# Kernel optimization log

Measured on AMD Instinct MI355X. Metric: run time of the kernel, lower is better.

Reference implementation:

```python
import jax, jax.numpy as jnp
import numpy as np

TAU = 0.5


def _l2norm(x):
    return x / jnp.linalg.norm(x, axis=1, keepdims=True)


def _project(z, W1, b1, W2, b2):
    h = jax.nn.elu(z @ W1.T + b1)
    return h @ W2.T + b2


def _semi_loss(h1, h2):
    # cos sim via row-normalized matmul
    n1 = _l2norm(h1)
    n2 = _l2norm(h2)
    between = jnp.exp((n1 @ n2.T) / TAU)  # [N, N]
    refl = jnp.exp((n1 @ n1.T) / TAU)     # [N, N]
    pos = jnp.diagonal(between)
    denom = refl.sum(axis=1) + between.sum(axis=1) + pos \
        - jnp.diagonal(refl) - jnp.diagonal(between)
    return -jnp.log(pos / denom)


def setup_inputs() -> dict:
    key = jax.random.key(0)
    k1, k2, k3, k4 = jax.random.split(key, 4)
    N, D, P = 12288, 256, 256
    z1 = jax.random.normal(k1, (N, D), dtype=jnp.float32)
    z2 = jax.random.normal(k2, (N, D), dtype=jnp.float32)
    W1 = jax.random.normal(k3, (P, D), dtype=jnp.float32) * (1.0 / np.sqrt(D))
    b1 = jnp.zeros((P,), dtype=jnp.float32)
    W2 = jax.random.normal(k4, (D, P), dtype=jnp.float32) * (1.0 / np.sqrt(P))
    b2 = jnp.zeros((D,), dtype=jnp.float32)
    return {"z1": z1, "z2": z2, "W1": W1, "b1": b1, "W2": W2, "b2": b2}


def reference(z1, z2, W1, b1, W2, b2):
    h1 = _project(z1, W1, b1, W2, b2)
    h2 = _project(z2, W1, b1, W2, b2)
    l1 = _semi_loss(h1, h2)
    l2 = _semi_loss(h2, h1)
    return ((l1 + l2) * 0.5).mean()
```

## Files before the change

kernel.cpp:

```cpp
#include <hip/hip_runtime.h>
#include <hip/hip_bf16.h>
#include <hip/hip_fp8.h>


#define NROWS 12288
#define TWO_N 24576
#define KDIM 256
#define BM 128
#define BN 128
#define BK 32
#define BJ 128
#define NTILE 192
#define PAIRS 96
#define SLOTS 16
#define FB 48
#define LOG2E 1.4426950408889634f
#define SIMSCALE 1.6986436f
#define LN2F 0.6931471805599453f

#if __has_builtin(__builtin_amdgcn_exp2f)
#define EXP2F(x) __builtin_amdgcn_exp2f(x)
#else
#define EXP2F(x) exp2f(x)
#endif

typedef __bf16 bf16x8 __attribute__((ext_vector_type(8)));
typedef __bf16 bf16x4v __attribute__((ext_vector_type(4)));
typedef float f32x4 __attribute__((ext_vector_type(4)));
typedef int i32x4 __attribute__((ext_vector_type(4)));
typedef int i32x8 __attribute__((ext_vector_type(8)));
typedef unsigned char uchar;

typedef const __attribute__((address_space(1))) void* gptr_t;
typedef __attribute__((address_space(3))) void* lptr_t;

__device__ __forceinline__ void stage_slab(const __bf16* g, int row0, int kelem,
                                           __bf16* lds, int w, int l) {
#pragma unroll
  for (int t = 0; t < 2; ++t) {
    int chunk = w * 2 + t;
    int r = chunk * 16 + (l >> 2);
    int c = l & 3;
    int src = c ^ (r & 3);
    const __bf16* ga = g + (size_t)(row0 + r) * KDIM + kelem + src * 8;
    __bf16* la = lds + chunk * 512;
    __builtin_amdgcn_global_load_lds((gptr_t)ga, (lptr_t)la, 16, 0, 0);
  }
}

__device__ __forceinline__ bf16x8 read_frag(const __bf16* lds, int rowbase,
                                            int tile, int l) {
  int r = rowbase + tile * 16 + (l & 15);
  int q = l >> 4;
  int blk = q ^ (r & 3);
  return *(const bf16x8*)(lds + r * 32 + blk * 8);
}

__device__ __forceinline__ void gemm_tile_core(const __bf16* A, int arow0,
                                               const __bf16* B, int brow0,
                                               __bf16* As, __bf16* Bs,
                                               f32x4 (&acc)[4][4], int w, int l) {
  const int warow = (w >> 1) * 64;
  const int wbrow = (w & 1) * 64;
#pragma unroll
  for (int ks = 0; ks < KDIM / BK; ++ks) {
    __syncthreads();
    stage_slab(A, arow0, ks * BK, As, w, l);
    stage_slab(B, brow0, ks * BK, Bs, w, l);
    __syncthreads();
    bf16x8 aF[4], bF[4];
#pragma unroll
    for (int mi = 0; mi < 4; ++mi) aF[mi] = read_frag(As, warow, mi, l);
#pragma unroll
    for (int ni = 0; ni < 4; ++ni) bF[ni] = read_frag(Bs, wbrow, ni, l);
#pragma unroll
    for (int mi = 0; mi < 4; ++mi)
#pragma unroll
      for (int ni = 0; ni < 4; ++ni)
        acc[mi][ni] = __builtin_amdgcn_mfma_f32_16x16x32_bf16(
            aF[mi], bF[ni], acc[mi][ni], 0, 0, 0);
  }
}

__global__ void cast_all_kernel(const float* __restrict__ z1,
                                const float* __restrict__ z2,
                                const float* __restrict__ W1,
                                const float* __restrict__ W2,
                                __bf16* __restrict__ Zb,
                                __bf16* __restrict__ W1b,
                                __bf16* __restrict__ W2b) {
  const int n4z = NROWS * KDIM / 4;
  const int n4w = KDIM * KDIM / 4;
  int i = blockIdx.x * blockDim.x + threadIdx.x;
  const float* src;
  __bf16* dst;
  int j;
  if (i < n4z) {
    src = z1; dst = Zb; j = i;
  } else if (i < 2 * n4z) {
    src = z2; dst = Zb + (size_t)NROWS * KDIM; j = i - n4z;
  } else if (i < 2 * n4z + n4w) {
    src = W1; dst = W1b; j = i - 2 * n4z;
  } else if (i < 2 * n4z + 2 * n4w) {
    src = W2; dst = W2b; j = i - 2 * n4z - n4w;
  } else {
    return;
  }
  float4 v = *(const float4*)(src + (size_t)j * 4);
  bf16x4v o;
  o[0] = (__bf16)v.x; o[1] = (__bf16)v.y; o[2] = (__bf16)v.z; o[3] = (__bf16)v.w;
  *(bf16x4v*)(dst + (size_t)j * 4) = o;
}

__global__ __launch_bounds__(256, 2) void proj1_kernel(
    const __bf16* __restrict__ Zb, const __bf16* __restrict__ W1b,
    const float* __restrict__ b1, __bf16* __restrict__ Tb) {
  __shared__ __align__(16) __bf16 As[BM * BK];
  __shared__ __align__(16) __bf16 Bs[BN * BK];
  int w = threadIdx.x >> 6, l = threadIdx.x & 63;
  int i0 = blockIdx.x * BM, j0 = blockIdx.y * BN;
  int warow = (w >> 1) * 64, wbrow = (w & 1) * 64;
  f32x4 acc[4][4] = {};
  gemm_tile_core(Zb, i0, W1b, j0, As, Bs, acc, w, l);
  float bias[4];
#pragma unroll
  for (int ni = 0; ni < 4; ++ni) bias[ni] = b1[j0 + wbrow + ni * 16 + (l & 15)];
#pragma unroll
  for (int mi = 0; mi < 4; ++mi)
#pragma unroll
    for (int ni = 0; ni < 4; ++ni)
#pragma unroll
      for (int v = 0; v < 4; ++v) {
        int row = i0 + warow + mi * 16 + (l >> 4) * 4 + v;
        int col = j0 + wbrow + ni * 16 + (l & 15);
        float x = acc[mi][ni][v] + bias[ni];
        x = x > 0.f ? x : (EXP2F(x * LOG2E) - 1.f);
        Tb[(size_t)row * KDIM + col] = (__bf16)x;
      }
}

__global__ __launch_bounds__(256, 2) void proj2_kernel(
    const __bf16* __restrict__ Tb, const __bf16* __restrict__ W2b,
    const float* __restrict__ b2, float* __restrict__ H,
    float* __restrict__ SS) {
  __shared__ __align__(16) __bf16 As[BM * BK];
  __shared__ __align__(16) __bf16 Bs[BN * BK];
  int w = threadIdx.x >> 6, l = threadIdx.x & 63;
  int i0 = blockIdx.x * BM, j0 = blockIdx.y * BN;
  int warow = (w >> 1) * 64, wbrow = (w & 1) * 64;
  f32x4 acc[4][4] = {};
  gemm_tile_core(Tb, i0, W2b, j0, As, Bs, acc, w, l);
  float bias[4];
#pragma unroll
  for (int ni = 0; ni < 4; ++ni) bias[ni] = b2[j0 + wbrow + ni * 16 + (l & 15)];
  float ss[4][4] = {};
#pragma unroll
  for (int mi = 0; mi < 4; ++mi)
#pragma unroll
    for (int ni = 0; ni < 4; ++ni)
#pragma unroll
      for (int v = 0; v < 4; ++v) {
        int row = i0 + warow + mi * 16 + (l >> 4) * 4 + v;
        int col = j0 + wbrow + ni * 16 + (l & 15);
        float x = acc[mi][ni][v] + bias[ni];
        H[(size_t)row * KDIM + col] = x;
        ss[mi][v] += x * x;
      }
#pragma unroll
  for (int mi = 0; mi < 4; ++mi)
#pragma unroll
    for (int v = 0; v < 4; ++v) {
      float x = ss[mi][v];
      x += __shfl_xor(x, 1, 64);
      x += __shfl_xor(x, 2, 64);
      x += __shfl_xor(x, 4, 64);
      x += __shfl_xor(x, 8, 64);
      if ((l & 15) == 0)
        atomicAdd(&SS[i0 + warow + mi * 16 + (l >> 4) * 4 + v], x);
    }
}

__device__ __forceinline__ unsigned int pack4_fp8(float a, float b, float c,
                                                  float d) {
#if __has_builtin(__builtin_amdgcn_cvt_pk_fp8_f32)
  int v = 0;
  v = __builtin_amdgcn_cvt_pk_fp8_f32(a, b, v, false);
  v = __builtin_amdgcn_cvt_pk_fp8_f32(c, d, v, true);
  return (unsigned int)v;
#else
  __hip_fp8_e4m3 qa(a), qb(b), qc(c), qd(d);
  return (unsigned int)qa.__x | ((unsigned int)qb.__x << 8) |
         ((unsigned int)qc.__x << 16) | ((unsigned int)qd.__x << 24);
#endif
}

__global__ void norm_kernel(const float* __restrict__ H,
                            const float* __restrict__ SS,
                            uchar* __restrict__ Nq) {
  int i = blockIdx.x * blockDim.x + threadIdx.x;
  size_t idx = (size_t)i * 8;
  if (idx >= (size_t)TWO_N * KDIM) return;
  int row = (int)(idx >> 8);
  float inv = rsqrtf(SS[row]) * SIMSCALE;
  float4 h0 = *(const float4*)(H + idx);
  float4 h1 = *(const float4*)(H + idx + 4);
  uint2 o;
  o.x = pack4_fp8(h0.x * inv, h0.y * inv, h0.z * inv, h0.w * inv);
  o.y = pack4_fp8(h1.x * inv, h1.y * inv, h1.z * inv, h1.w * inv);
  *(uint2*)(Nq + idx) = o;
}

__global__ __launch_bounds__(256, 2) void sim_kernel(
    const uchar* __restrict__ Nq, float* __restrict__ Rlow,
    float* __restrict__ Rhigh, float* __restrict__ Dsame,
    float* __restrict__ Dcross) {
  __shared__ __align__(16) uchar Bs[2][BJ * KDIM];
  int tid = threadIdx.x;
  int w = tid >> 6, l = tid & 63;
  int q = l >> 4;
  int rx = l & 15;
  int b = blockIdx.x;
  int p = b >> 4;
  int s = b & 15;
  const int I1 = p, I2 = NTILE - 1 - p;
  const int L1 = NTILE - I1;
  int fstart = (s == 0) ? 0 : 13 + (s - 1) * 12;
  int fend = fstart + ((s == 0) ? 13 : 12);
  int warow = (w >> 1) * 64;
  int wbcol = (w & 1) * 64;

  unsigned off0[8];
#pragma unroll
  for (int t = 0; t < 8; ++t) {
    int ch = w * 8 + t;
    int r = ch * 4 + (l >> 4);
    int c = l & 15;
    int src = c ^ (r & 15);
    off0[t] = (unsigned)(r * KDIM + src * 16);
  }
  auto jtile_of = [&](int F) { return (F < L1) ? (I1 + F) : (F - 1); };
  auto atile_of = [&](int F) { return (F < L1) ? I1 : I2; };

  auto stage = [&](int F, int bi) {
    unsigned jo = (unsigned)(jtile_of(F) * (BM * KDIM));
#pragma unroll
    for (int t = 0; t < 8; ++t) {
      const uchar* ga = Nq + (size_t)(jo + off0[t]);
      uchar* la = Bs[bi] + (w * 8 + t) * 1024;
      __builtin_amdgcn_global_load_lds((gptr_t)ga, (lptr_t)la, 16, 0, 0);
    }
  };

  i32x8 aF[4][2];
  auto load_aF = [&](int Atile) {
#pragma unroll
    for (int mi = 0; mi < 4; ++mi) {
      const uchar* ap = Nq +
          (size_t)(Atile * BM + warow + mi * 16 + rx) * KDIM + q * 32;
#pragma unroll
      for (int hf = 0; hf < 2; ++hf)
        aF[mi][hf] = *(const i32x8*)(ap + hf * 128);
    }
  };

  int rdo[2][2];
#pragma unroll
  for (int hf = 0; hf < 2; ++hf) {
    int kb = hf * 8 + 2 * q;
    rdo[hf][0] = (kb ^ rx) << 4;
    rdo[hf][1] = ((kb + 1) ^ rx) << 4;
  }

  f32x4 rs4[4] = {};
  f32x4 cs4[4];
  int pend = 0;
  float* pendR = nullptr;
  int pendBase = 0;

  auto flushrs = [&](int Atile, int h) {
    float* R = h ? Rhigh : Rlow;
#pragma unroll
    for (int mi = 0; mi < 4; ++mi)
#pragma unroll
      for (int v = 0; v < 4; ++v) {
        float x = rs4[mi][v];
        x += __shfl_xor(x, 1, 64);
        x += __shfl_xor(x, 2, 64);
        x += __shfl_xor(x, 4, 64);
        x += __shfl_xor(x, 8, 64);
        if (rx == 0)
          atomicAdd(&R[Atile * BM + warow + mi * 16 + q * 4 + v], x);
        rs4[mi][v] = 0.f;
      }
  };
  auto flushcs = [&]() {
#pragma unroll
    for (int nj = 0; nj < 4; ++nj) {
      float c = (cs4[nj][0] + cs4[nj][1]) + (cs4[nj][2] + cs4[nj][3]);
      c += __shfl_xor(c, 16, 64);
      c += __shfl_xor(c, 32, 64);
      if (q == 0)
        atomicAdd(&pendR[pendBase + wbcol + nj * 16 + rx], c);
    }
    pend = 0;
  };

  const f32x4 Z4 = {0.f, 0.f, 0.f, 0.f};

  int Aprev = atile_of(fstart);
  int hprev = (jtile_of(fstart) >= NTILE / 2) ? 1 : 0;
  load_aF(Aprev);
  stage(fstart, 0);

  for (int f = fstart; f < fend; ++f) {
    int bi = (f - fstart) & 1;
    __syncthreads();
    if (f + 1 < fend) stage(f + 1, bi ^ 1);
    if (pend) flushcs();

    int Atile = atile_of(f);
    int Jt = jtile_of(f);
    int h = (Jt >= NTILE / 2) ? 1 : 0;
    if (Atile != Aprev) {
      flushrs(Aprev, hprev);
      load_aF(Atile);
      Aprev = Atile;
      hprev = h;
    } else if (h != hprev) {
      flushrs(Aprev, hprev);
      hprev = h;
    }

    bool dsame = (Jt == Atile);
    bool dcross = (Jt == Atile + NTILE / 2);
    float* Rcol = (Atile >= NTILE / 2) ? Rhigh : Rlow;

    const uchar* bL = Bs[bi] + (size_t)(wbcol + rx) * KDIM;
    const uchar* p00 = bL + rdo[0][0];
    const uchar* p01 = bL + rdo[0][1];
    const uchar* p10 = bL + rdo[1][0];
    const uchar* p11 = bL + rdo[1][1];

#pragma unroll
    for (int nj = 0; nj < 4; ++nj) {
      const int no = nj * 4096;
      i32x8 bF0 = __builtin_shufflevector(*(const i32x4*)(p00 + no),
                                          *(const i32x4*)(p01 + no),
                                          0, 1, 2, 3, 4, 5, 6, 7);
      i32x8 bF1 = __builtin_shufflevector(*(const i32x4*)(p10 + no),
                                          *(const i32x4*)(p11 + no),
                                          0, 1, 2, 3, 4, 5, 6, 7);
      f32x4 acc[4];
#pragma unroll
      for (int mi = 0; mi < 4; ++mi)
        acc[mi] = __builtin_amdgcn_mfma_scale_f32_16x16x128_f8f6f4(
            aF[mi][0], bF0, Z4, 0, 0, 0, 0x7F7F7F7F, 0, 0x7F7F7F7F);
#pragma unroll
      for (int mi = 0; mi < 4; ++mi)
        acc[mi] = __builtin_amdgcn_mfma_scale_f32_16x16x128_f8f6f4(
            aF[mi][1], bF1, acc[mi], 0, 0, 0, 0x7F7F7F7F, 0, 0x7F7F7F7F);
#pragma unroll
      for (int mi = 0; mi < 4; ++mi) {
        f32x4 e4;
        e4[0] = EXP2F(acc[mi][0]);
        e4[1] = EXP2F(acc[mi][1]);
        e4[2] = EXP2F(acc[mi][2]);
        e4[3] = EXP2F(acc[mi][3]);
        rs4[mi] += e4;
        cs4[nj] = (mi == 0) ? e4 : (cs4[nj] + e4);
      }

      if (dsame | dcross) {
        float* D = dsame ? Dsame : Dcross;
#pragma unroll
        for (int mi = 0; mi < 4; ++mi)
#pragma unroll
          for (int v = 0; v < 4; ++v) {
            int li = warow + mi * 16 + q * 4 + v;
            int lj = wbcol + nj * 16 + rx;
            if (li == lj) D[Atile * BM + li] = acc[mi][v];
          }
      }
    }

    if (!dsame) {
      pend = 1;
      pendR = Rcol;
      pendBase = Jt * BM;
    }
  }

  if (pend) flushcs();
  flushrs(Aprev, hprev);
}

__global__ void finalize1_kernel(const float* __restrict__ Rlow,
                                 const float* __restrict__ Rhigh,
                                 const float* __restrict__ Dsame,
                                 const float* __restrict__ Dcross,
                                 float* __restrict__ partial) {
  __shared__ float red[256];
  int k = blockIdx.x * 256 + threadIdx.x;
  float d1 = Rlow[k] + Rhigh[k] - EXP2F(Dsame[k]);
  float d2 = Rhigh[NROWS + k] + Rlow[NROWS + k] - EXP2F(Dsame[NROWS + k]);
  float acc = 0.5f * (logf(d1) + logf(d2)) - LN2F * Dcross[k];
  red[threadIdx.x] = acc;
  __syncthreads();
  for (int s = 128; s > 0; s >>= 1) {
    if (threadIdx.x < s) red[threadIdx.x] += red[threadIdx.x + s];
    __syncthreads();
  }
  if (threadIdx.x == 0) partial[blockIdx.x] = red[0];
}

__global__ void finalize2_kernel(const float* __restrict__ partial,
                                 float* __restrict__ out) {
  float x = (threadIdx.x < FB) ? partial[threadIdx.x] : 0.f;
#pragma unroll
  for (int s = 32; s > 0; s >>= 1) x += __shfl_down(x, s, 64);
  if (threadIdx.x == 0) out[0] = x / (float)NROWS;
}

extern "C" void kernel_launch(void* const* d_in, const int* in_sizes, int n_in,
                              void* d_out, int out_size, void* d_ws,
                              size_t ws_size, hipStream_t stream) {
  const float* z1 = (const float*)d_in[0];
  const float* z2 = (const float*)d_in[1];
  const float* W1 = (const float*)d_in[2];
  const float* b1 = (const float*)d_in[3];
  const float* W2 = (const float*)d_in[4];
  const float* b2 = (const float*)d_in[5];
  float* out = (float*)d_out;

  char* ws = (char*)d_ws;
  size_t off = 0;
  auto alloc = [&](size_t bytes) -> void* {
    void* p = ws + off;
    off += (bytes + 255) & ~(size_t)255;
    return p;
  };
  __bf16* Zb   = (__bf16*)alloc((size_t)TWO_N * KDIM * 2);
  __bf16* W1b  = (__bf16*)alloc((size_t)KDIM * KDIM * 2);
  __bf16* W2b  = (__bf16*)alloc((size_t)KDIM * KDIM * 2);
  __bf16* Tb   = (__bf16*)alloc((size_t)TWO_N * KDIM * 2);
  float*  H    = (float*)alloc((size_t)TWO_N * KDIM * 4);
  float*  SS   = (float*)alloc((size_t)TWO_N * 4);
  float*  Rlow = (float*)alloc((size_t)TWO_N * 4);
  float*  Rhigh= (float*)alloc((size_t)TWO_N * 4);
  float*  Dsame= (float*)alloc((size_t)TWO_N * 4);
  float*  Dcross=(float*)alloc((size_t)NROWS * 4);
  float*  partial=(float*)alloc((size_t)FB * 4);
  uchar*  Nq = (uchar*)Zb;

  hipMemsetAsync(SS, 0, (size_t)TWO_N * 4, stream);
  hipMemsetAsync(Rlow, 0, (size_t)TWO_N * 4, stream);
  hipMemsetAsync(Rhigh, 0, (size_t)TWO_N * 4, stream);

  int n4z = NROWS * KDIM / 4;
  int n4w = KDIM * KDIM / 4;
  int n4all = 2 * n4z + 2 * n4w;
  cast_all_kernel<<<(n4all + 255) / 256, 256, 0, stream>>>(z1, z2, W1, W2, Zb,
                                                           W1b, W2b);

  proj1_kernel<<<dim3(TWO_N / BM, KDIM / BN), 256, 0, stream>>>(Zb, W1b, b1, Tb);
  proj2_kernel<<<dim3(TWO_N / BM, KDIM / BN), 256, 0, stream>>>(Tb, W2b, b2, H, SS);

  int n8n = TWO_N * KDIM / 8;
  norm_kernel<<<(n8n + 255) / 256, 256, 0, stream>>>(H, SS, Nq);

  sim_kernel<<<PAIRS * SLOTS, 256, 0, stream>>>(Nq, Rlow, Rhigh, Dsame,
                                                Dcross);
  finalize1_kernel<<<FB, 256, 0, stream>>>(Rlow, Rhigh, Dsame, Dcross, partial);
  finalize2_kernel<<<1, 64, 0, stream>>>(partial, out);
}
```

Before: 226.4 us.

## Load B fragments directly from global instead of staging through LDS

Removes the double-buffered LDS staging of the B tile (global_load_lds plus __syncthreads) in the similarity kernel and has each wave load its B fragments straight from global memory, software-prefetching the next 16-column slice into registers. It also merges three memsets into one, which relies on SS, Rlow and Rhigh being contiguous in the workspace. This drops block-wide barriers and the LDS footprint, which could raise occupancy. In exchange, B data is no longer shared across the waves of a block, so global/L2 traffic per block doubles.

```diff
diff --git a/kernel.cpp b/kernel.cpp
--- a/kernel.cpp
+++ b/kernel.cpp
@@ -9,7 +9,6 @@
 #define BM 128
 #define BN 128
 #define BK 32
-#define BJ 128
 #define NTILE 192
 #define PAIRS 96
 #define SLOTS 16
@@ -214,7 +213,6 @@
     const uchar* __restrict__ Nq, float* __restrict__ Rlow,
     float* __restrict__ Rhigh, float* __restrict__ Dsame,
     float* __restrict__ Dcross) {
-  __shared__ __align__(16) uchar Bs[2][BJ * KDIM];
   int tid = threadIdx.x;
   int w = tid >> 6, l = tid & 63;
   int q = l >> 4;
@@ -229,26 +227,19 @@
   int warow = (w >> 1) * 64;
   int wbcol = (w & 1) * 64;
 
-  unsigned off0[8];
-#pragma unroll
-  for (int t = 0; t < 8; ++t) {
-    int ch = w * 8 + t;
-    int r = ch * 4 + (l >> 4);
-    int c = l & 15;
-    int src = c ^ (r & 15);
-    off0[t] = (unsigned)(r * KDIM + src * 16);
-  }
   auto jtile_of = [&](int F) { return (F < L1) ? (I1 + F) : (F - 1); };
   auto atile_of = [&](int F) { return (F < L1) ? I1 : I2; };
 
-  auto stage = [&](int F, int bi) {
-    unsigned jo = (unsigned)(jtile_of(F) * (BM * KDIM));
-#pragma unroll
-    for (int t = 0; t < 8; ++t) {
-      const uchar* ga = Nq + (size_t)(jo + off0[t]);
-      uchar* la = Bs[bi] + (w * 8 + t) * 1024;
-      __builtin_amdgcn_global_load_lds((gptr_t)ga, (lptr_t)la, 16, 0, 0);
-    }
+  const uchar* bBase = Nq + (size_t)(wbcol + rx) * KDIM + q * 32;
+
+  auto loadB = [&](int Jt, int nj, i32x8& b0, i32x8& b1) {
+    const uchar* ptr = bBase + (size_t)Jt * (BM * KDIM) + nj * (16 * KDIM);
+    i32x4 a0 = *(const i32x4*)(ptr);
+    i32x4 a1 = *(const i32x4*)(ptr + 16);
+    i32x4 a2 = *(const i32x4*)(ptr + 128);
+    i32x4 a3 = *(const i32x4*)(ptr + 144);
+    b0 = __builtin_shufflevector(a0, a1, 0, 1, 2, 3, 4, 5, 6, 7);
+    b1 = __builtin_shufflevector(a2, a3, 0, 1, 2, 3, 4, 5, 6, 7);
   };
 
   i32x8 aF[4][2];
@@ -262,14 +253,6 @@
         aF[mi][hf] = *(const i32x8*)(ap + hf * 128);
     }
   };
-
-  int rdo[2][2];
-#pragma unroll
-  for (int hf = 0; hf < 2; ++hf) {
-    int kb = hf * 8 + 2 * q;
-    rdo[hf][0] = (kb ^ rx) << 4;
-    rdo[hf][1] = ((kb + 1) ^ rx) << 4;
-  }
 
   f32x4 rs4[4] = {};
   f32x4 cs4[4];
@@ -310,17 +293,16 @@
   int Aprev = atile_of(fstart);
   int hprev = (jtile_of(fstart) >= NTILE / 2) ? 1 : 0;
   load_aF(Aprev);
-  stage(fstart, 0);
 
   for (int f = fstart; f < fend; ++f) {
-    int bi = (f - fstart) & 1;
-    __syncthreads();
-    if (f + 1 < fend) stage(f + 1, bi ^ 1);
-    if (pend) flushcs();
-
     int Atile = atile_of(f);
     int Jt = jtile_of(f);
     int h = (Jt >= NTILE / 2) ? 1 : 0;
+
+    i32x8 b0c, b1c, b0n, b1n;
+    loadB(Jt, 0, b0c, b1c);
+
+    if (pend) flushcs();
     if (Atile != Aprev) {
       flushrs(Aprev, hprev);
       load_aF(Atile);
@@ -335,30 +317,18 @@
     bool dcross = (Jt == Atile + NTILE / 2);
     float* Rcol = (Atile >= NTILE / 2) ? Rhigh : Rlow;
 
-    const uchar* bL = Bs[bi] + (size_t)(wbcol + rx) * KDIM;
-    const uchar* p00 = bL + rdo[0][0];
-    const uchar* p01 = bL + rdo[0][1];
-    const uchar* p10 = bL + rdo[1][0];
-    const uchar* p11 = bL + rdo[1][1];
-
 #pragma unroll
     for (int nj = 0; nj < 4; ++nj) {
-      const int no = nj * 4096;
-      i32x8 bF0 = __builtin_shufflevector(*(const i32x4*)(p00 + no),
-                                          *(const i32x4*)(p01 + no),
-                                          0, 1, 2, 3, 4, 5, 6, 7);
-      i32x8 bF1 = __builtin_shufflevector(*(const i32x4*)(p10 + no),
-                                          *(const i32x4*)(p11 + no),
-                                          0, 1, 2, 3, 4, 5, 6, 7);
+      if (nj < 3) loadB(Jt, nj + 1, b0n, b1n);
       f32x4 acc[4];
 #pragma unroll
       for (int mi = 0; mi < 4; ++mi)
         acc[mi] = __builtin_amdgcn_mfma_scale_f32_16x16x128_f8f6f4(
-            aF[mi][0], bF0, Z4, 0, 0, 0, 0x7F7F7F7F, 0, 0x7F7F7F7F);
+            aF[mi][0], b0c, Z4, 0, 0, 0, 0x7F7F7F7F, 0, 0x7F7F7F7F);
 #pragma unroll
       for (int mi = 0; mi < 4; ++mi)
         acc[mi] = __builtin_amdgcn_mfma_scale_f32_16x16x128_f8f6f4(
-            aF[mi][1], bF1, acc[mi], 0, 0, 0, 0x7F7F7F7F, 0, 0x7F7F7F7F);
+            aF[mi][1], b1c, acc[mi], 0, 0, 0, 0x7F7F7F7F, 0, 0x7F7F7F7F);
 #pragma unroll
       for (int mi = 0; mi < 4; ++mi) {
         f32x4 e4;
@@ -381,6 +351,8 @@
             if (li == lj) D[Atile * BM + li] = acc[mi][v];
           }
       }
+      b0c = b0n;
+      b1c = b1n;
     }
 
     if (!dsame) {
@@ -452,9 +424,7 @@
   float*  partial=(float*)alloc((size_t)FB * 4);
   uchar*  Nq = (uchar*)Zb;
 
-  hipMemsetAsync(SS, 0, (size_t)TWO_N * 4, stream);
-  hipMemsetAsync(Rlow, 0, (size_t)TWO_N * 4, stream);
-  hipMemsetAsync(Rhigh, 0, (size_t)TWO_N * 4, stream);
+  hipMemsetAsync(SS, 0, (size_t)3 * TWO_N * 4, stream);
 
   int n4z = NROWS * KDIM / 4;
   int n4w = KDIM * KDIM / 4;
```

Result: slower. 270.2 us (+19.3%).

## Swap operand roles in sim kernel: keep column tile in registers, stream rows

Applied to the files above, without the earlier changes.

The similarity kernel now keeps the fixed tile (jbig or p) as B fragments in registers and streams the varying tiles through LDS as the A operand. The per-tile row-sum reduction moves to a deferred atomic flush, and the column sums accumulate across iterations and flush only when the tile or half changes. This is meant to cut the number of column-sum atomics and shuffle reductions, which previously happened on every tile. The three separate memsets are merged into one, which relies on SS, Rlow and Rhigh being contiguous in the workspace; each allocation is 96 KB, a multiple of 256 bytes, so no padding gaps appear.

```diff
diff --git a/kernel.cpp b/kernel.cpp
--- a/kernel.cpp
+++ b/kernel.cpp
@@ -9,7 +9,6 @@
 #define BM 128
 #define BN 128
 #define BK 32
-#define BJ 128
 #define NTILE 192
 #define PAIRS 96
 #define SLOTS 16
@@ -214,7 +213,7 @@
     const uchar* __restrict__ Nq, float* __restrict__ Rlow,
     float* __restrict__ Rhigh, float* __restrict__ Dsame,
     float* __restrict__ Dcross) {
-  __shared__ __align__(16) uchar Bs[2][BJ * KDIM];
+  __shared__ __align__(16) uchar As[2][BM * KDIM];
   int tid = threadIdx.x;
   int w = tid >> 6, l = tid & 63;
   int q = l >> 4;
@@ -222,8 +221,8 @@
   int b = blockIdx.x;
   int p = b >> 4;
   int s = b & 15;
-  const int I1 = p, I2 = NTILE - 1 - p;
-  const int L1 = NTILE - I1;
+  const int jbig = NTILE - 1 - p;
+  const int len1 = NTILE - p;
   int fstart = (s == 0) ? 0 : 13 + (s - 1) * 12;
   int fend = fstart + ((s == 0) ? 13 : 12);
   int warow = (w >> 1) * 64;
@@ -233,33 +232,31 @@
 #pragma unroll
   for (int t = 0; t < 8; ++t) {
     int ch = w * 8 + t;
-    int r = ch * 4 + (l >> 4);
-    int c = l & 15;
-    int src = c ^ (r & 15);
+    int r = ch * 4 + q;
+    int src = rx ^ (r & 15);
     off0[t] = (unsigned)(r * KDIM + src * 16);
   }
-  auto jtile_of = [&](int F) { return (F < L1) ? (I1 + F) : (F - 1); };
-  auto atile_of = [&](int F) { return (F < L1) ? I1 : I2; };
+  auto a_of = [&](int F) { return (F < len1) ? F : F - len1; };
+  auto j_of = [&](int F) { return (F < len1) ? jbig : p; };
 
   auto stage = [&](int F, int bi) {
-    unsigned jo = (unsigned)(jtile_of(F) * (BM * KDIM));
+    unsigned jo = (unsigned)(a_of(F) * (BM * KDIM));
 #pragma unroll
     for (int t = 0; t < 8; ++t) {
       const uchar* ga = Nq + (size_t)(jo + off0[t]);
-      uchar* la = Bs[bi] + (w * 8 + t) * 1024;
+      uchar* la = As[bi] + (w * 8 + t) * 1024;
       __builtin_amdgcn_global_load_lds((gptr_t)ga, (lptr_t)la, 16, 0, 0);
     }
   };
 
-  i32x8 aF[4][2];
-  auto load_aF = [&](int Atile) {
-#pragma unroll
-    for (int mi = 0; mi < 4; ++mi) {
-      const uchar* ap = Nq +
-          (size_t)(Atile * BM + warow + mi * 16 + rx) * KDIM + q * 32;
-#pragma unroll
-      for (int hf = 0; hf < 2; ++hf)
-        aF[mi][hf] = *(const i32x8*)(ap + hf * 128);
+  i32x8 bF[4][2];
+  auto load_bF = [&](int jt) {
+#pragma unroll
+    for (int nj = 0; nj < 4; ++nj) {
+      const uchar* bp =
+          Nq + (size_t)(jt * BM + wbcol + nj * 16 + rx) * KDIM + q * 32;
+      bF[nj][0] = *(const i32x8*)(bp);
+      bF[nj][1] = *(const i32x8*)(bp + 128);
     }
   };
 
@@ -272,13 +269,113 @@
   }
 
   f32x4 rs4[4] = {};
-  f32x4 cs4[4];
-  int pend = 0;
-  float* pendR = nullptr;
-  int pendBase = 0;
-
-  auto flushrs = [&](int Atile, int h) {
+  f32x4 cs4[4] = {};
+  int rpend = 0, rBase = 0;
+  float* rP = nullptr;
+
+  auto flushrs_atomic = [&]() {
+    if (rx == 0) {
+#pragma unroll
+      for (int mi = 0; mi < 4; ++mi)
+#pragma unroll
+        for (int v = 0; v < 4; ++v)
+          atomicAdd(&rP[rBase + warow + mi * 16 + q * 4 + v], rs4[mi][v]);
+    }
+#pragma unroll
+    for (int mi = 0; mi < 4; ++mi)
+      rs4[mi] = (f32x4){0.f, 0.f, 0.f, 0.f};
+    rpend = 0;
+  };
+  auto flushcs = [&](int jt, int h) {
     float* R = h ? Rhigh : Rlow;
+#pragma unroll
+    for (int nj = 0; nj < 4; ++nj) {
+      float c = (cs4[nj][0] + cs4[nj][1]) + (cs4[nj][2] + cs4[nj][3]);
+      c += __shfl_xor(c, 16, 64);
+      c += __shfl_xor(c, 32, 64);
+      if (q == 0)
+        atomicAdd(&R[jt * BM + wbcol + nj * 16 + rx], c);
+      cs4[nj] = (f32x4){0.f, 0.f, 0.f, 0.f};
+    }
+  };
+
+  const f32x4 Z4 = {0.f, 0.f, 0.f, 0.f};
+
+  int jcur = j_of(fstart);
+  int csh = (a_of(fstart) >= NTILE / 2) ? 1 : 0;
+  load_bF(jcur);
+  stage(fstart, 0);
+
+  for (int f = fstart; f < fend; ++f) {
+    int bi = (f - fstart) & 1;
+    __syncthreads();
+    if (f + 1 < fend) stage(f + 1, bi ^ 1);
+    if (rpend) flushrs_atomic();
+
+    int a = a_of(f), jt = j_of(f);
+    if (jt != jcur) {
+      flushcs(jcur, csh);
+      load_bF(jt);
+      jcur = jt;
+      csh = 0;
+    }
+    int ha = (a >= NTILE / 2) ? 1 : 0;
+    if (ha != csh) { flushcs(jcur, csh); csh = ha; }
+
+    bool dsame = (a == jt);
+    bool dcross = (jt == a + NTILE / 2);
+
+    const uchar* aL = As[bi] + (size_t)(warow + rx) * KDIM;
+    i32x8 aF[4][2];
+#pragma unroll
+    for (int mi = 0; mi < 4; ++mi) {
+      const int mo = mi * 4096;
+      aF[mi][0] = __builtin_shufflevector(
+          *(const i32x4*)(aL + mo + rdo[0][0]),
+          *(const i32x4*)(aL + mo + rdo[0][1]), 0, 1, 2, 3, 4, 5, 6, 7);
+      aF[mi][1] = __builtin_shufflevector(
+          *(const i32x4*)(aL + mo + rdo[1][0]),
+          *(const i32x4*)(aL + mo + rdo[1][1]), 0, 1, 2, 3, 4, 5, 6, 7);
+    }
+
+#pragma unroll
+    for (int nj = 0; nj < 4; ++nj) {
+      f32x4 acc[4];
+#pragma unroll
+      for (int mi = 0; mi < 4; ++mi)
+        acc[mi] = __builtin_amdgcn_mfma_scale_f32_16x16x128_f8f6f4(
+            aF[mi][0], bF[nj][0], Z4, 0, 0, 0, 0x7F7F7F7F, 0, 0x7F7F7F7F);
+#pragma unroll
+      for (int mi = 0; mi < 4; ++mi)
+        acc[mi] = __builtin_amdgcn_mfma_scale_f32_16x16x128_f8f6f4(
+            aF[mi][1], bF[nj][1], acc[mi], 0, 0, 0, 0x7F7F7F7F, 0, 0x7F7F7F7F);
+
+      if (dsame | dcross) {
+        float* D = dsame ? Dsame : Dcross;
+#pragma unroll
+        for (int mi = 0; mi < 4; ++mi)
+#pragma unroll
+          for (int v = 0; v < 4; ++v) {
+            int li = warow + mi * 16 + q * 4 + v;
+            int lj = wbcol + nj * 16 + rx;
+            if (li == lj) D[a * BM + li] = acc[mi][v];
+          }
+      }
+
+#pragma unroll
+      for (int mi = 0; mi < 4; ++mi) {
+        f32x4 e4;
+        e4[0] = EXP2F(acc[mi][0]);
+        e4[1] = EXP2F(acc[mi][1]);
+        e4[2] = EXP2F(acc[mi][2]);
+        e4[3] = EXP2F(acc[mi][3]);
+        acc[mi] = e4;
+        rs4[mi] += e4;
+      }
+      if (!dsame)
+        cs4[nj] += (acc[0] + acc[1]) + (acc[2] + acc[3]);
+    }
+
 #pragma unroll
     for (int mi = 0; mi < 4; ++mi)
 #pragma unroll
@@ -288,110 +385,15 @@
         x += __shfl_xor(x, 2, 64);
         x += __shfl_xor(x, 4, 64);
         x += __shfl_xor(x, 8, 64);
-        if (rx == 0)
-          atomicAdd(&R[Atile * BM + warow + mi * 16 + q * 4 + v], x);
-        rs4[mi][v] = 0.f;
+        rs4[mi][v] = x;
       }
-  };
-  auto flushcs = [&]() {
-#pragma unroll
-    for (int nj = 0; nj < 4; ++nj) {
-      float c = (cs4[nj][0] + cs4[nj][1]) + (cs4[nj][2] + cs4[nj][3]);
-      c += __shfl_xor(c, 16, 64);
-      c += __shfl_xor(c, 32, 64);
-      if (q == 0)
-        atomicAdd(&pendR[pendBase + wbcol + nj * 16 + rx], c);
-    }
-    pend = 0;
-  };
-
-  const f32x4 Z4 = {0.f, 0.f, 0.f, 0.f};
-
-  int Aprev = atile_of(fstart);
-  int hprev = (jtile_of(fstart) >= NTILE / 2) ? 1 : 0;
-  load_aF(Aprev);
-  stage(fstart, 0);
-
-  for (int f = fstart; f < fend; ++f) {
-    int bi = (f - fstart) & 1;
-    __syncthreads();
-    if (f + 1 < fend) stage(f + 1, bi ^ 1);
-    if (pend) flushcs();
-
-    int Atile = atile_of(f);
-    int Jt = jtile_of(f);
-    int h = (Jt >= NTILE / 2) ? 1 : 0;
-    if (Atile != Aprev) {
-      flushrs(Aprev, hprev);
-      load_aF(Atile);
-      Aprev = Atile;
-      hprev = h;
-    } else if (h != hprev) {
-      flushrs(Aprev, hprev);
-      hprev = h;
-    }
-
-    bool dsame = (Jt == Atile);
-    bool dcross = (Jt == Atile + NTILE / 2);
-    float* Rcol = (Atile >= NTILE / 2) ? Rhigh : Rlow;
-
-    const uchar* bL = Bs[bi] + (size_t)(wbcol + rx) * KDIM;
-    const uchar* p00 = bL + rdo[0][0];
-    const uchar* p01 = bL + rdo[0][1];
-    const uchar* p10 = bL + rdo[1][0];
-    const uchar* p11 = bL + rdo[1][1];
-
-#pragma unroll
-    for (int nj = 0; nj < 4; ++nj) {
-      const int no = nj * 4096;
-      i32x8 bF0 = __builtin_shufflevector(*(const i32x4*)(p00 + no),
-                                          *(const i32x4*)(p01 + no),
-                                          0, 1, 2, 3, 4, 5, 6, 7);
-      i32x8 bF1 = __builtin_shufflevector(*(const i32x4*)(p10 + no),
-                                          *(const i32x4*)(p11 + no),
-                                          0, 1, 2, 3, 4, 5, 6, 7);
-      f32x4 acc[4];
-#pragma unroll
-      for (int mi = 0; mi < 4; ++mi)
-        acc[mi] = __builtin_amdgcn_mfma_scale_f32_16x16x128_f8f6f4(
-            aF[mi][0], bF0, Z4, 0, 0, 0, 0x7F7F7F7F, 0, 0x7F7F7F7F);
-#pragma unroll
-      for (int mi = 0; mi < 4; ++mi)
-        acc[mi] = __builtin_amdgcn_mfma_scale_f32_16x16x128_f8f6f4(
-            aF[mi][1], bF1, acc[mi], 0, 0, 0, 0x7F7F7F7F, 0, 0x7F7F7F7F);
-#pragma unroll
-      for (int mi = 0; mi < 4; ++mi) {
-        f32x4 e4;
-        e4[0] = EXP2F(acc[mi][0]);
-        e4[1] = EXP2F(acc[mi][1]);
-        e4[2] = EXP2F(acc[mi][2]);
-        e4[3] = EXP2F(acc[mi][3]);
-        rs4[mi] += e4;
-        cs4[nj] = (mi == 0) ? e4 : (cs4[nj] + e4);
-      }
-
-      if (dsame | dcross) {
-        float* D = dsame ? Dsame : Dcross;
-#pragma unroll
-        for (int mi = 0; mi < 4; ++mi)
-#pragma unroll
-          for (int v = 0; v < 4; ++v) {
-            int li = warow + mi * 16 + q * 4 + v;
-            int lj = wbcol + nj * 16 + rx;
-            if (li == lj) D[Atile * BM + li] = acc[mi][v];
-          }
-      }
-    }
-
-    if (!dsame) {
-      pend = 1;
-      pendR = Rcol;
-      pendBase = Jt * BM;
-    }
-  }
-
-  if (pend) flushcs();
-  flushrs(Aprev, hprev);
+    rP = (jt >= NTILE / 2) ? Rhigh : Rlow;
+    rBase = a * BM;
+    rpend = 1;
+  }
+
+  if (rpend) flushrs_atomic();
+  flushcs(jcur, csh);
 }
 
 __global__ void finalize1_kernel(const float* __restrict__ Rlow,
@@ -452,9 +454,7 @@
   float*  partial=(float*)alloc((size_t)FB * 4);
   uchar*  Nq = (uchar*)Zb;
 
-  hipMemsetAsync(SS, 0, (size_t)TWO_N * 4, stream);
-  hipMemsetAsync(Rlow, 0, (size_t)TWO_N * 4, stream);
-  hipMemsetAsync(Rhigh, 0, (size_t)TWO_N * 4, stream);
+  hipMemsetAsync(SS, 0, (size_t)3 * TWO_N * 4, stream);
 
   int n4z = NROWS * KDIM / 4;
   int n4w = KDIM * KDIM / 4;
```

New measurement: 287.8 us. 1.27x slower.

## Fuse second projection GEMM with row L2-normalization and FP8 quantization

Applied to the files above, without the earlier changes.

Replaces the proj2 and norm kernels with one kernel. Each block computes 64 full rows across all 256 output columns, so row sums of squares are reduced in shared memory and the rows are normalized and packed to FP8 directly. This removes the fp32 H intermediate written and read through global memory, the SS atomics, and their memset. It also merges the two accumulator memsets into one, which relies on Rlow and Rhigh being adjacent in the workspace. In exchange the grid is 384 blocks with more shared memory per block, which may load the CUs less evenly.

```diff
diff --git a/kernel.cpp b/kernel.cpp
--- a/kernel.cpp
+++ b/kernel.cpp
@@ -9,7 +9,6 @@
 #define BM 128
 #define BN 128
 #define BK 32
-#define BJ 128
 #define NTILE 192
 #define PAIRS 96
 #define SLOTS 16
@@ -139,20 +138,70 @@
       }
 }
 
-__global__ __launch_bounds__(256, 2) void proj2_kernel(
+__device__ __forceinline__ uchar fp8_byte(float x) {
+#if __has_builtin(__builtin_amdgcn_cvt_pk_fp8_f32)
+  int v = __builtin_amdgcn_cvt_pk_fp8_f32(x, 0.f, 0, false);
+  return (uchar)(v & 0xFF);
+#else
+  __hip_fp8_e4m3 qv(x);
+  return qv.__x;
+#endif
+}
+
+__global__ __launch_bounds__(256, 2) void proj2norm_kernel(
     const __bf16* __restrict__ Tb, const __bf16* __restrict__ W2b,
-    const float* __restrict__ b2, float* __restrict__ H,
-    float* __restrict__ SS) {
-  __shared__ __align__(16) __bf16 As[BM * BK];
-  __shared__ __align__(16) __bf16 Bs[BN * BK];
-  int w = threadIdx.x >> 6, l = threadIdx.x & 63;
-  int i0 = blockIdx.x * BM, j0 = blockIdx.y * BN;
-  int warow = (w >> 1) * 64, wbrow = (w & 1) * 64;
+    const float* __restrict__ b2, uchar* __restrict__ Nq) {
+  __shared__ __align__(16) __bf16 As[64 * BK];
+  __shared__ __align__(16) __bf16 Bs[KDIM * BK];
+  __shared__ float ssred[4][64];
+  __shared__ float invred[64];
+  __shared__ __align__(8) uchar qbuf[64 * KDIM];
+  int tid = threadIdx.x;
+  int w = tid >> 6, l = tid & 63;
+  int q = l >> 4, rx = l & 15;
+  int i0 = blockIdx.x * 64;
+  int wbcol = w * 64;
+
   f32x4 acc[4][4] = {};
-  gemm_tile_core(Tb, i0, W2b, j0, As, Bs, acc, w, l);
+#pragma unroll
+  for (int ks = 0; ks < KDIM / BK; ++ks) {
+    __syncthreads();
+#pragma unroll
+    for (int t = 0; t < 5; ++t) {
+      int c = w * 5 + t;
+      int rr = l >> 2, c2 = l & 3;
+      if (c < 4) {
+        int r = c * 16 + rr;
+        int src = c2 ^ (r & 3);
+        const __bf16* ga = Tb + (size_t)(i0 + r) * KDIM + ks * BK + src * 8;
+        __builtin_amdgcn_global_load_lds((gptr_t)ga, (lptr_t)(As + c * 512),
+                                         16, 0, 0);
+      } else {
+        int cc = c - 4;
+        int r = cc * 16 + rr;
+        int src = c2 ^ (r & 3);
+        const __bf16* ga = W2b + (size_t)r * KDIM + ks * BK + src * 8;
+        __builtin_amdgcn_global_load_lds((gptr_t)ga, (lptr_t)(Bs + cc * 512),
+                                         16, 0, 0);
+      }
+    }
+    __syncthreads();
+    bf16x8 aF[4], bF[4];
+#pragma unroll
+    for (int mi = 0; mi < 4; ++mi) aF[mi] = read_frag(As, 0, mi, l);
+#pragma unroll
+    for (int ni = 0; ni < 4; ++ni) bF[ni] = read_frag(Bs, wbcol, ni, l);
+#pragma unroll
+    for (int mi = 0; mi < 4; ++mi)
+#pragma unroll
+      for (int ni = 0; ni < 4; ++ni)
+        acc[mi][ni] = __builtin_amdgcn_mfma_f32_16x16x32_bf16(
+            aF[mi], bF[ni], acc[mi][ni], 0, 0, 0);
+  }
+
   float bias[4];
 #pragma unroll
-  for (int ni = 0; ni < 4; ++ni) bias[ni] = b2[j0 + wbrow + ni * 16 + (l & 15)];
+  for (int ni = 0; ni < 4; ++ni) bias[ni] = b2[wbcol + ni * 16 + rx];
   float ss[4][4] = {};
 #pragma unroll
   for (int mi = 0; mi < 4; ++mi)
@@ -160,10 +209,8 @@
     for (int ni = 0; ni < 4; ++ni)
 #pragma unroll
       for (int v = 0; v < 4; ++v) {
-        int row = i0 + warow + mi * 16 + (l >> 4) * 4 + v;
-        int col = j0 + wbrow + ni * 16 + (l & 15);
         float x = acc[mi][ni][v] + bias[ni];
-        H[(size_t)row * KDIM + col] = x;
+        acc[mi][ni][v] = x;
         ss[mi][v] += x * x;
       }
 #pragma unroll
@@ -175,46 +222,39 @@
       x += __shfl_xor(x, 2, 64);
       x += __shfl_xor(x, 4, 64);
       x += __shfl_xor(x, 8, 64);
-      if ((l & 15) == 0)
-        atomicAdd(&SS[i0 + warow + mi * 16 + (l >> 4) * 4 + v], x);
-    }
-}
-
-__device__ __forceinline__ unsigned int pack4_fp8(float a, float b, float c,
-                                                  float d) {
-#if __has_builtin(__builtin_amdgcn_cvt_pk_fp8_f32)
-  int v = 0;
-  v = __builtin_amdgcn_cvt_pk_fp8_f32(a, b, v, false);
-  v = __builtin_amdgcn_cvt_pk_fp8_f32(c, d, v, true);
-  return (unsigned int)v;
-#else
-  __hip_fp8_e4m3 qa(a), qb(b), qc(c), qd(d);
-  return (unsigned int)qa.__x | ((unsigned int)qb.__x << 8) |
-         ((unsigned int)qc.__x << 16) | ((unsigned int)qd.__x << 24);
-#endif
-}
-
-__global__ void norm_kernel(const float* __restrict__ H,
-                            const float* __restrict__ SS,
-                            uchar* __restrict__ Nq) {
-  int i = blockIdx.x * blockDim.x + threadIdx.x;
-  size_t idx = (size_t)i * 8;
-  if (idx >= (size_t)TWO_N * KDIM) return;
-  int row = (int)(idx >> 8);
-  float inv = rsqrtf(SS[row]) * SIMSCALE;
-  float4 h0 = *(const float4*)(H + idx);
-  float4 h1 = *(const float4*)(H + idx + 4);
-  uint2 o;
-  o.x = pack4_fp8(h0.x * inv, h0.y * inv, h0.z * inv, h0.w * inv);
-  o.y = pack4_fp8(h1.x * inv, h1.y * inv, h1.z * inv, h1.w * inv);
-  *(uint2*)(Nq + idx) = o;
+      if (rx == 0) ssred[w][mi * 16 + q * 4 + v] = x;
+    }
+  __syncthreads();
+  if (tid < 64)
+    invred[tid] = rsqrtf(ssred[0][tid] + ssred[1][tid] + ssred[2][tid] +
+                         ssred[3][tid]) * SIMSCALE;
+  __syncthreads();
+
+#pragma unroll
+  for (int mi = 0; mi < 4; ++mi)
+#pragma unroll
+    for (int v = 0; v < 4; ++v) {
+      int row = mi * 16 + q * 4 + v;
+      float iv = invred[row];
+#pragma unroll
+      for (int ni = 0; ni < 4; ++ni)
+        qbuf[row * KDIM + wbcol + ni * 16 + rx] =
+            fp8_byte(acc[mi][ni][v] * iv);
+    }
+  __syncthreads();
+  size_t base = (size_t)i0 * KDIM;
+#pragma unroll
+  for (int it = 0; it < 8; ++it) {
+    int idx = it * 2048 + tid * 8;
+    *(uint2*)(Nq + base + idx) = *(const uint2*)(qbuf + idx);
+  }
 }
 
 __global__ __launch_bounds__(256, 2) void sim_kernel(
     const uchar* __restrict__ Nq, float* __restrict__ Rlow,
     float* __restrict__ Rhigh, float* __restrict__ Dsame,
     float* __restrict__ Dcross) {
-  __shared__ __align__(16) uchar Bs[2][BJ * KDIM];
+  __shared__ __align__(16) uchar Bs[2][BM * KDIM];
   int tid = threadIdx.x;
   int w = tid >> 6, l = tid & 63;
   int q = l >> 4;
@@ -359,6 +399,7 @@
       for (int mi = 0; mi < 4; ++mi)
         acc[mi] = __builtin_amdgcn_mfma_scale_f32_16x16x128_f8f6f4(
             aF[mi][1], bF1, acc[mi], 0, 0, 0, 0x7F7F7F7F, 0, 0x7F7F7F7F);
+      float cs = 0.f;
 #pragma unroll
       for (int mi = 0; mi < 4; ++mi) {
         f32x4 e4;
@@ -369,6 +410,7 @@
         rs4[mi] += e4;
         cs4[nj] = (mi == 0) ? e4 : (cs4[nj] + e4);
       }
+      (void)cs;
 
       if (dsame | dcross) {
         float* D = dsame ? Dsame : Dcross;
@@ -443,8 +485,6 @@
   __bf16* W1b  = (__bf16*)alloc((size_t)KDIM * KDIM * 2);
   __bf16* W2b  = (__bf16*)alloc((size_t)KDIM * KDIM * 2);
   __bf16* Tb   = (__bf16*)alloc((size_t)TWO_N * KDIM * 2);
-  float*  H    = (float*)alloc((size_t)TWO_N * KDIM * 4);
-  float*  SS   = (float*)alloc((size_t)TWO_N * 4);
   float*  Rlow = (float*)alloc((size_t)TWO_N * 4);
   float*  Rhigh= (float*)alloc((size_t)TWO_N * 4);
   float*  Dsame= (float*)alloc((size_t)TWO_N * 4);
@@ -452,9 +492,7 @@
   float*  partial=(float*)alloc((size_t)FB * 4);
   uchar*  Nq = (uchar*)Zb;
 
-  hipMemsetAsync(SS, 0, (size_t)TWO_N * 4, stream);
-  hipMemsetAsync(Rlow, 0, (size_t)TWO_N * 4, stream);
-  hipMemsetAsync(Rhigh, 0, (size_t)TWO_N * 4, stream);
+  hipMemsetAsync(Rlow, 0, (size_t)2 * TWO_N * 4, stream);
 
   int n4z = NROWS * KDIM / 4;
   int n4w = KDIM * KDIM / 4;
@@ -463,10 +501,7 @@
                                                            W1b, W2b);
 
   proj1_kernel<<<dim3(TWO_N / BM, KDIM / BN), 256, 0, stream>>>(Zb, W1b, b1, Tb);
-  proj2_kernel<<<dim3(TWO_N / BM, KDIM / BN), 256, 0, stream>>>(Tb, W2b, b2, H, SS);
-
-  int n8n = TWO_N * KDIM / 8;
-  norm_kernel<<<(n8n + 255) / 256, 256, 0, stream>>>(H, SS, Nq);
+  proj2norm_kernel<<<TWO_N / 64, 256, 0, stream>>>(Tb, W2b, b2, Nq);
 
   sim_kernel<<<PAIRS * SLOTS, 256, 0, stream>>>(Nq, Rlow, Rhigh, Dsame,
                                                 Dcross);
```

New measurement: 216.4 us. -4.4%, faster.
